# Kernel optimization log

Measured on AMD Instinct MI355X. Metric: run time of the kernel, lower is better.

The kernel has to match this reference:

```python
import jax, jax.numpy as jnp
import numpy as np

LN_EPS = 1e-5

def _ln(x, g, b):
    mu = x.mean(-1, keepdims=True)
    var = ((x - mu) ** 2).mean(-1, keepdims=True)
    return (x - mu) * jax.lax.rsqrt(var + LN_EPS) * g + b

def _gru(x, h, wih, whh, bih, bhh):
    # torch GRUCell: gates ordered (r, z, n)
    gi = x @ wih.T + bih
    gh = h @ whh.T + bhh
    ir, iz, inn = jnp.split(gi, 3, axis=-1)
    hr, hz, hn = jnp.split(gh, 3, axis=-1)
    r = jax.nn.sigmoid(ir + hr)
    z = jax.nn.sigmoid(iz + hz)
    n = jnp.tanh(inn + r * hn)
    return (1.0 - z) * n + z * h

def setup_inputs() -> dict:
    key = jax.random.key(0)
    ks = jax.random.split(key, 10)
    B, N, D, S, H = 64, 4096, 128, 8, 256
    w = D ** -0.5  # weight scale to keep activations sane
    return {
        'inputs': jax.random.normal(ks[0], (B, N, D), jnp.float32),
        'slot_noise': jax.random.normal(ks[1], (1, S, D), jnp.float32),
        'slots_mu': jax.random.normal(ks[2], (1, S, D), jnp.float32) * w,
        'slots_log_sigma': jnp.zeros((1, S, D), jnp.float32),
        'wq': jax.random.normal(ks[3], (D, D), jnp.float32) * w,
        'bq': jnp.zeros((D,), jnp.float32),
        'wk': jax.random.normal(ks[4], (D, D), jnp.float32) * w,
        'bk': jnp.zeros((D,), jnp.float32),
        'wv': jax.random.normal(ks[5], (D, D), jnp.float32) * w,
        'bv': jnp.zeros((D,), jnp.float32),
        'gru_wih': jax.random.normal(ks[6], (3 * D, D), jnp.float32) * w,
        'gru_whh': jax.random.normal(ks[7], (3 * D, D), jnp.float32) * w,
        'gru_bih': jnp.zeros((3 * D,), jnp.float32),
        'gru_bhh': jnp.zeros((3 * D,), jnp.float32),
        'ns_g': jnp.ones((D,), jnp.float32),
        'ns_b': jnp.zeros((D,), jnp.float32),
        'ni_g': jnp.ones((D,), jnp.float32),
        'ni_b': jnp.zeros((D,), jnp.float32),
        'mlp_ln_g': jnp.ones((D,), jnp.float32),
        'mlp_ln_b': jnp.zeros((D,), jnp.float32),
        'mlp_w1': jax.random.normal(ks[8], (H, D), jnp.float32) * w,
        'mlp_b1': jnp.zeros((H,), jnp.float32),
        'mlp_w2': jax.random.normal(ks[9], (D, H), jnp.float32) * (H ** -0.5),
        'mlp_b2': jnp.zeros((D,), jnp.float32),
    }

N_ITERS = 3

def reference(inputs, slot_noise, slots_mu, slots_log_sigma, wq, bq, wk, bk, wv, bv,
              gru_wih, gru_whh, gru_bih, gru_bhh, ns_g, ns_b, ni_g, ni_b,
              mlp_ln_g, mlp_ln_b, mlp_w1, mlp_b1, mlp_w2, mlp_b2):
    B, N, D = inputs.shape
    S = slots_mu.shape[1]
    slots = slots_mu + jnp.exp(slots_log_sigma) * slot_noise  # [1,S,D]
    slots = jnp.broadcast_to(slots, (B, S, D))
    x = _ln(inputs, ni_g, ni_b)
    k = x @ wk.T + bk  # [B,N,D]
    v = x @ wv.T + bv
    scale = 1.0 / jnp.sqrt(jnp.float32(D))
    for _ in range(N_ITERS):
        q = _ln(slots, ns_g, ns_b) @ wq.T + bq  # [B,S,D]
        logits = jnp.einsum('bnd,bsd->bns', k, q) * scale
        attn = jax.nn.softmax(logits, axis=-1)  # softmax over slots
        attn_norm = jnp.clip(attn.sum(axis=1, keepdims=True), 1e-8, None)
        slot_attn = attn / attn_norm
        updates = jnp.einsum('bns,bnd->bsd', slot_attn, v)
        slots = _gru(updates, slots, gru_wih, gru_whh, gru_bih, gru_bhh)
        h = jax.nn.gelu(_ln(slots, mlp_ln_g, mlp_ln_b) @ mlp_w1.T + mlp_b1, approximate=False)
        slots = slots + (h @ mlp_w2.T + mlp_b2)
    return slots
```

## Files before the change

### kernel.cpp

```cpp
#include <hip/hip_runtime.h>
#include <hip/hip_bf16.h>
#include <math.h>

#define Bn 64
#define Nn 4096
#define Dn 128
#define Sn 8
#define Hn 256
#define LN_EPS 1e-5f
#define QSCALE 0.08838834764831845f
#define NCHUNK 16

typedef __bf16 bf16x8 __attribute__((ext_vector_type(8)));
typedef float f32x4 __attribute__((ext_vector_type(4)));
typedef unsigned short ushort_t;

__device__ __forceinline__ float dot4(float4 a, float4 b) {
    return a.x*b.x + a.y*b.y + a.z*b.z + a.w*b.w;
}
__device__ __forceinline__ ushort_t f2bf(float f) {
    __bf16 b = (__bf16)f;
    ushort_t u; __builtin_memcpy(&u, &b, 2); return u;
}
__device__ __forceinline__ bf16x8 zero8() {
    bf16x8 z;
    #pragma unroll
    for (int i = 0; i < 8; ++i) z[i] = (__bf16)0.0f;
    return z;
}

__global__ void k_prep(const float* __restrict__ wk, const float* __restrict__ wv,
                       ushort_t* __restrict__ wallT,
                       const float* __restrict__ mu, const float* __restrict__ ls,
                       const float* __restrict__ noise, float* __restrict__ slots) {
    if (blockIdx.x < 128) {
        int o = blockIdx.x * 256 + threadIdx.x;
        int e = o & 7;
        int l = (o >> 3) & 15;
        int q = (o >> 7) & 3;
        int k = (o >> 9) & 3;
        int G = o >> 11;
        int row = G * 16 + l;
        int col = k * 32 + q * 8 + e;
        float f = (row < 128) ? wk[row * 128 + col] : wv[(row - 128) * 128 + col];
        wallT[o] = f2bf(f);
    } else {
        int i = (blockIdx.x - 128) * 256 + threadIdx.x;
        if (i < Sn * Dn) {
            float v = mu[i] + __expf(ls[i]) * noise[i];
            #pragma unroll 4
            for (int b = 0; b < Bn; ++b) slots[b * Sn * Dn + i] = v;
        }
    }
}

__global__ __launch_bounds__(512) void k_lnkv_mfma(
    const float* __restrict__ inp, const float* __restrict__ ni_g, const float* __restrict__ ni_b,
    const ushort_t* __restrict__ wallT, const float* __restrict__ bk, const float* __restrict__ bv,
    ushort_t* __restrict__ kout, ushort_t* __restrict__ vout)
{
    __shared__ ushort_t wsh[32768];
    const int t = threadIdx.x;
    const int lane = t & 63;
    const int w = t >> 6;
    const int l15 = lane & 15, q = lane >> 4;
    const int rowbase = blockIdx.x * 128;
    const int row = rowbase + w * 16 + l15;
    const int b_idx = rowbase >> 12;

    const float* xr = inp + (size_t)row * Dn + q * 8;
    float4 xv[8];
    #pragma unroll
    for (int c = 0; c < 4; ++c) {
        xv[2*c]   = *(const float4*)(xr + c * 32);
        xv[2*c+1] = *(const float4*)(xr + c * 32 + 4);
    }
    #pragma unroll
    for (int i = 0; i < 8; ++i) {
        int off = (i * 512 + t) * 8;
        *(bf16x8*)&wsh[off] = *(const bf16x8*)&wallT[off];
    }

    float s = 0.f, sq = 0.f;
    #pragma unroll
    for (int i = 0; i < 8; ++i) {
        float4 x4 = xv[i];
        s  += x4.x + x4.y + x4.z + x4.w;
        sq += x4.x*x4.x + x4.y*x4.y + x4.z*x4.z + x4.w*x4.w;
    }
    s  += __shfl_xor(s, 16);  s  += __shfl_xor(s, 32);
    sq += __shfl_xor(sq, 16); sq += __shfl_xor(sq, 32);
    float mu = s * (1.0f / 128.0f);
    float rs = rsqrtf(sq * (1.0f / 128.0f) - mu * mu + LN_EPS);

    bf16x8 xf[4];
    #pragma unroll
    for (int c = 0; c < 4; ++c) {
        const float* gp = ni_g + c * 32 + q * 8;
        const float* bp = ni_b + c * 32 + q * 8;
        float4 g0 = *(const float4*)gp, g1 = *(const float4*)(gp + 4);
        float4 b0 = *(const float4*)bp, b1 = *(const float4*)(bp + 4);
        bf16x8 f;
        f[0] = (__bf16)((xv[2*c].x   - mu) * rs * g0.x + b0.x);
        f[1] = (__bf16)((xv[2*c].y   - mu) * rs * g0.y + b0.y);
        f[2] = (__bf16)((xv[2*c].z   - mu) * rs * g0.z + b0.z);
        f[3] = (__bf16)((xv[2*c].w   - mu) * rs * g0.w + b0.w);
        f[4] = (__bf16)((xv[2*c+1].x - mu) * rs * g1.x + b1.x);
        f[5] = (__bf16)((xv[2*c+1].y - mu) * rs * g1.y + b1.y);
        f[6] = (__bf16)((xv[2*c+1].z - mu) * rs * g1.z + b1.z);
        f[7] = (__bf16)((xv[2*c+1].w - mu) * rs * g1.w + b1.w);
        xf[c] = f;
    }

    __syncthreads();

    const int nloc0 = (rowbase & 4095) + w * 16 + q * 4;
    #pragma unroll
    for (int ct = 0; ct < 16; ++ct) {
        bf16x8 af[4];
        #pragma unroll
        for (int k4 = 0; k4 < 4; ++k4)
            af[k4] = *(const bf16x8*)&wsh[((ct * 4 + k4) * 64 + lane) * 8];
        f32x4 acc = {0.f, 0.f, 0.f, 0.f};
        if (ct < 8) {
            #pragma unroll
            for (int k4 = 0; k4 < 4; ++k4)
                acc = __builtin_amdgcn_mfma_f32_16x16x32_bf16(af[k4], xf[k4], acc, 0, 0, 0);
            int d0 = ct * 16 + q * 4;
            float4 bia = *(const float4*)&bk[d0];
            ushort4 o = { f2bf(acc[0] + bia.x), f2bf(acc[1] + bia.y),
                          f2bf(acc[2] + bia.z), f2bf(acc[3] + bia.w) };
            size_t off = ((size_t)(((rowbase >> 4) + w) * 4 + (d0 >> 5)) * 64
                          + ((d0 >> 3) & 3) * 16 + l15) * 8 + (d0 & 7);
            *(ushort4*)&kout[off] = o;
        } else {
            #pragma unroll
            for (int k4 = 0; k4 < 4; ++k4)
                acc = __builtin_amdgcn_mfma_f32_16x16x32_bf16(xf[k4], af[k4], acc, 0, 0, 0);
            int dgrp = ct - 8;
            float bb = bv[dgrp * 16 + l15];
            ushort4 o = { f2bf(acc[0] + bb), f2bf(acc[1] + bb),
                          f2bf(acc[2] + bb), f2bf(acc[3] + bb) };
            size_t off = (((size_t)(b_idx * 8 + dgrp) * 128 + (nloc0 >> 5)) * 64
                          + ((nloc0 >> 3) & 3) * 16 + l15) * 8 + (nloc0 & 7);
            *(ushort4*)&vout[off] = o;
        }
    }
}

__global__ __launch_bounds__(256) void k_qproj2(
    const float* __restrict__ slots, const float* __restrict__ ns_g, const float* __restrict__ ns_b,
    const float* __restrict__ wq, const float* __restrict__ bq,
    ushort_t* __restrict__ qb)
{
    __shared__ float lnq[8][128];
    const int t = threadIdx.x;
    const int bs0 = blockIdx.x * 8;
    {
        int r = t >> 5, c = (t & 31) * 4;
        float4 x4 = *(const float4*)&slots[(size_t)(bs0 + r) * Dn + c];
        float s  = x4.x + x4.y + x4.z + x4.w;
        float sq = x4.x*x4.x + x4.y*x4.y + x4.z*x4.z + x4.w*x4.w;
        #pragma unroll
        for (int m = 1; m <= 16; m <<= 1) { s += __shfl_xor(s, m); sq += __shfl_xor(sq, m); }
        float mu = s * (1.0f / 128.0f);
        float rs = rsqrtf(sq * (1.0f / 128.0f) - mu * mu + LN_EPS);
        lnq[r][c+0] = (x4.x - mu) * rs * ns_g[c+0] + ns_b[c+0];
        lnq[r][c+1] = (x4.y - mu) * rs * ns_g[c+1] + ns_b[c+1];
        lnq[r][c+2] = (x4.z - mu) * rs * ns_g[c+2] + ns_b[c+2];
        lnq[r][c+3] = (x4.w - mu) * rs * ns_g[c+3] + ns_b[c+3];
    }
    __syncthreads();
    {
        int c = t & 127, rb = (t >> 7) * 4;
        const float* W = wq + (size_t)c * Dn;
        float acc[4] = {0.f, 0.f, 0.f, 0.f};
        for (int d = 0; d < 128; d += 4) {
            float4 w4 = *(const float4*)(W + d);
            #pragma unroll
            for (int rr = 0; rr < 4; ++rr) acc[rr] += dot4(w4, *(const float4*)&lnq[rb + rr][d]);
        }
        float bb = bq[c];
        #pragma unroll
        for (int rr = 0; rr < 4; ++rr)
            qb[(size_t)(bs0 + rb + rr) * Dn + c] = f2bf((acc[rr] + bb) * QSCALE);
    }
}

__global__ __launch_bounds__(512) void k_attn_mfma(
    const ushort_t* __restrict__ kbuf, const ushort_t* __restrict__ vtbuf,
    const ushort_t* __restrict__ qb,
    float* __restrict__ upart, float* __restrict__ npart)
{
    __shared__ float ush[8][8][128];
    __shared__ float nsh[8][8];
    __shared__ ushort_t psh[8][8][32];
    const int t = threadIdx.x;
    const int b = blockIdx.y;
    const int chunk = blockIdx.x;
    const int lane = t & 63;
    const int w = t >> 6;
    const int l15 = lane & 15, q = lane >> 4;

    bf16x8 aq[4];
    #pragma unroll
    for (int c = 0; c < 4; ++c) {
        bf16x8 z = zero8();
        if (l15 < 8)
            z = *(const bf16x8*)&qb[((size_t)b * Sn + l15) * Dn + c * 32 + q * 8];
        aq[c] = z;
    }

    const int n32 = chunk * 256 + w * 32;
    const int ng = n32 >> 4;
    const int nc = n32 >> 5;

    f32x4 lg2[2];
    #pragma unroll
    for (int T = 0; T < 2; ++T) {
        f32x4 lg = {0.f, 0.f, 0.f, 0.f};
        #pragma unroll
        for (int c = 0; c < 4; ++c) {
            bf16x8 kf = *(const bf16x8*)&kbuf[(((size_t)b * 256 + ng + T) * 4 + c) * 512 + lane * 8];
            lg = __builtin_amdgcn_mfma_f32_16x16x32_bf16(aq[c], kf, lg, 0, 0, 0);
        }
        lg2[T] = lg;
    }

    bf16x8 bvf[8];
    #pragma unroll
    for (int dg = 0; dg < 8; ++dg)
        bvf[dg] = *(const bf16x8*)&vtbuf[(((size_t)b * 8 + dg) * 128 + nc) * 512 + lane * 8];

    #pragma unroll
    for (int T = 0; T < 2; ++T) {
        f32x4 lg = lg2[T];
        float m = fmaxf(fmaxf(lg[0], lg[1]), fmaxf(lg[2], lg[3]));
        m = fmaxf(m, __shfl_xor(m, 16));
        float e0 = __expf(lg[0] - m);
        float e1 = __expf(lg[1] - m);
        float e2 = __expf(lg[2] - m);
        float e3 = __expf(lg[3] - m);
        float ss = (e0 + e1) + (e2 + e3);
        ss += __shfl_xor(ss, 16);
        float inv = 1.0f / ss;
        if (q < 2) {
            psh[w][q * 4 + 0][T * 16 + l15] = f2bf(e0 * inv);
            psh[w][q * 4 + 1][T * 16 + l15] = f2bf(e1 * inv);
            psh[w][q * 4 + 2][T * 16 + l15] = f2bf(e2 * inv);
            psh[w][q * 4 + 3][T * 16 + l15] = f2bf(e3 * inv);
        }
    }

    bf16x8 pa = zero8();
    if (l15 < 8)
        pa = *(const bf16x8*)&psh[w][l15][q * 8];

    float nacc = 0.f;
    #pragma unroll
    for (int e = 0; e < 8; ++e) nacc += (float)pa[e];

    f32x4 acc[8];
    #pragma unroll
    for (int dg = 0; dg < 8; ++dg) {
        acc[dg] = (f32x4){0.f, 0.f, 0.f, 0.f};
        acc[dg] = __builtin_amdgcn_mfma_f32_16x16x32_bf16(pa, bvf[dg], acc[dg], 0, 0, 0);
    }

    nacc += __shfl_xor(nacc, 16);
    nacc += __shfl_xor(nacc, 32);
    if (lane < 8) nsh[w][lane] = nacc;
    if (q < 2) {
        #pragma unroll
        for (int dg = 0; dg < 8; ++dg)
            #pragma unroll
            for (int r = 0; r < 4; ++r)
                ush[w][q * 4 + r][dg * 16 + l15] = acc[dg][r];
    }
    __syncthreads();
    if (t < 256) {
        int s = t >> 5, d0 = (t & 31) * 4;
        float4 sum = {0.f, 0.f, 0.f, 0.f};
        #pragma unroll
        for (int w8 = 0; w8 < 8; ++w8) {
            float4 vv = *(const float4*)&ush[w8][s][d0];
            sum.x += vv.x; sum.y += vv.y; sum.z += vv.z; sum.w += vv.w;
        }
        *(float4*)&upart[((size_t)chunk * 512 + b * 8 + s) * 128 + d0] = sum;
    }
    if (t < 8) {
        float sn = 0.f;
        #pragma unroll
        for (int w8 = 0; w8 < 8; ++w8) sn += nsh[w8][t];
        npart[chunk * 512 + b * 8 + t] = sn;
    }
}

__global__ __launch_bounds__(512) void k_update3(
    const float* __restrict__ slots,
    const float* __restrict__ upart, const float* __restrict__ npart,
    const float* __restrict__ wih, const float* __restrict__ whh,
    const float* __restrict__ bih, const float* __restrict__ bhh,
    const float* __restrict__ mlg, const float* __restrict__ mlb,
    const float* __restrict__ w1, const float* __restrict__ b1,
    const float* __restrict__ w2, const float* __restrict__ b2,
    const float* __restrict__ ns_g, const float* __restrict__ ns_b,
    const float* __restrict__ wq, const float* __restrict__ bq,
    float* __restrict__ outp, ushort_t* __restrict__ qb, int do_q)
{
    __shared__ float us[128];
    __shared__ float hs[128];
    __shared__ float gs[768];
    __shared__ float hnw[128];
    __shared__ float lns[128];
    __shared__ float h1s[256];
    const int t = threadIdx.x;
    const int bs = blockIdx.x;

    if (t < 128) {
        float u = 0.f;
        #pragma unroll
        for (int c = 0; c < NCHUNK; ++c) u += upart[((size_t)(c * 512 + bs)) * 128 + t];
        float nsum = 0.f;
        #pragma unroll
        for (int c = 0; c < NCHUNK; ++c) nsum += npart[c * 512 + bs];
        us[t] = u / fmaxf(nsum, 1e-8f);
        hs[t] = slots[(size_t)bs * Dn + t];
    }
    __syncthreads();

    #pragma unroll
    for (int jj = 0; jj < 2; ++jj) {
        int j = t + jj * 512;
        if (jj == 0 || t < 256) {
            const float* W = (j < 384) ? (wih + (size_t)j * Dn) : (whh + (size_t)(j - 384) * Dn);
            const float* X = (j < 384) ? us : hs;
            float a = 0.f;
            #pragma unroll 8
            for (int d = 0; d < 128; d += 4)
                a += dot4(*(const float4*)(W + d), *(const float4*)(X + d));
            gs[j] = a;
        }
    }
    __syncthreads();

    if (t < 64) {
        float hnew[2];
        #pragma unroll
        for (int e = 0; e < 2; ++e) {
            int i = t + e * 64;
            float ir = gs[i]       + bih[i],       hr = gs[384 + i] + bhh[i];
            float iz = gs[128 + i] + bih[128 + i], hz = gs[512 + i] + bhh[128 + i];
            float in_= gs[256 + i] + bih[256 + i], hn = gs[640 + i] + bhh[256 + i];
            float r = 1.0f / (1.0f + __expf(-(ir + hr)));
            float z = 1.0f / (1.0f + __expf(-(iz + hz)));
            float n = tanhf(in_ + r * hn);
            hnew[e] = (1.0f - z) * n + z * hs[i];
        }
        float s  = hnew[0] + hnew[1];
        float sq = hnew[0]*hnew[0] + hnew[1]*hnew[1];
        #pragma unroll
        for (int m = 1; m <= 32; m <<= 1) { s += __shfl_xor(s, m); sq += __shfl_xor(sq, m); }
        float mu = s * (1.0f / 128.0f);
        float rs = rsqrtf(sq * (1.0f / 128.0f) - mu * mu + LN_EPS);
        #pragma unroll
        for (int e = 0; e < 2; ++e) {
            int i = t + e * 64;
            hnw[i] = hnew[e];
            lns[i] = (hnew[e] - mu) * rs * mlg[i] + mlb[i];
        }
    }
    __syncthreads();

    {
        int h = t >> 1, half = t & 1;
        const float* W = w1 + (size_t)h * Dn + half * 64;
        const float* X = lns + half * 64;
        float a = 0.f;
        #pragma unroll 8
        for (int d = 0; d < 64; d += 4)
            a += dot4(*(const float4*)(W + d), *(const float4*)(X + d));
        a += __shfl_xor(a, 1);
        if (half == 0) {
            float x = a + b1[h];
            h1s[h] = 0.5f * x * (1.0f + erff(x * 0.70710678118654752f));
        }
    }
    __syncthreads();

    {
        int d = t >> 2, q4 = t & 3;
        const float* W = w2 + (size_t)d * Hn + q4 * 64;
        const float* X = h1s + q4 * 64;
        float a = 0.f;
        #pragma unroll 8
        for (int e = 0; e < 64; e += 4)
            a += dot4(*(const float4*)(W + e), *(const float4*)(X + e));
        a += __shfl_xor(a, 1);
        a += __shfl_xor(a, 2);
        if (q4 == 0) {
            float o = hnw[d] + a + b2[d];
            outp[(size_t)bs * Dn + d] = o;
            us[d] = o;
        }
    }
    if (do_q) {
        __syncthreads();
        if (t < 64) {
            float v0 = us[t], v1 = us[t + 64];
            float s  = v0 + v1;
            float sq = v0*v0 + v1*v1;
            #pragma unroll
            for (int m = 1; m <= 32; m <<= 1) { s += __shfl_xor(s, m); sq += __shfl_xor(sq, m); }
            float mu = s * (1.0f / 128.0f);
            float rs = rsqrtf(sq * (1.0f / 128.0f) - mu * mu + LN_EPS);
            lns[t]      = (v0 - mu) * rs * ns_g[t]      + ns_b[t];
            lns[t + 64] = (v1 - mu) * rs * ns_g[t + 64] + ns_b[t + 64];
        }
        __syncthreads();
        {
            int d = t >> 2, q4 = t & 3;
            const float* W = wq + (size_t)d * Dn + q4 * 32;
            const float* X = lns + q4 * 32;
            float a = 0.f;
            #pragma unroll 8
            for (int e = 0; e < 32; e += 4)
                a += dot4(*(const float4*)(W + e), *(const float4*)(X + e));
            a += __shfl_xor(a, 1);
            a += __shfl_xor(a, 2);
            if (q4 == 0)
                qb[(size_t)bs * Dn + d] = f2bf((a + bq[d]) * QSCALE);
        }
    }
}

extern "C" void kernel_launch(void* const* d_in, const int* in_sizes, int n_in,
                              void* d_out, int out_size, void* d_ws, size_t ws_size,
                              hipStream_t stream) {
    (void)in_sizes; (void)n_in; (void)out_size; (void)ws_size;
    const float* inputs   = (const float*)d_in[0];
    const float* noise    = (const float*)d_in[1];
    const float* slots_mu = (const float*)d_in[2];
    const float* slots_ls = (const float*)d_in[3];
    const float* wq  = (const float*)d_in[4];
    const float* bq  = (const float*)d_in[5];
    const float* wk  = (const float*)d_in[6];
    const float* bk  = (const float*)d_in[7];
    const float* wv  = (const float*)d_in[8];
    const float* bv  = (const float*)d_in[9];
    const float* gwih = (const float*)d_in[10];
    const float* gwhh = (const float*)d_in[11];
    const float* gbih = (const float*)d_in[12];
    const float* gbhh = (const float*)d_in[13];
    const float* ns_g = (const float*)d_in[14];
    const float* ns_b = (const float*)d_in[15];
    const float* ni_g = (const float*)d_in[16];
    const float* ni_b = (const float*)d_in[17];
    const float* mlg  = (const float*)d_in[18];
    const float* mlb  = (const float*)d_in[19];
    const float* mw1  = (const float*)d_in[20];
    const float* mb1  = (const float*)d_in[21];
    const float* mw2  = (const float*)d_in[22];
    const float* mb2  = (const float*)d_in[23];

    float* ws      = (float*)d_ws;
    float* slots   = ws;
    float* upart   = ws + 65536;
    float* npart   = ws + 1114112;
    ushort_t* qb    = (ushort_t*)(ws + 1122304);
    ushort_t* wallT = (ushort_t*)(ws + 1155072);
    ushort_t* kbuf  = (ushort_t*)(ws + 1171456);
    ushort_t* vtbuf = kbuf + 33554432;

    k_prep<<<132, 256, 0, stream>>>(wk, wv, wallT, slots_mu, slots_ls, noise, slots);
    k_lnkv_mfma<<<2048, 512, 0, stream>>>(inputs, ni_g, ni_b, wallT, bk, bv, kbuf, vtbuf);
    k_qproj2<<<64, 256, 0, stream>>>(slots, ns_g, ns_b, wq, bq, qb);
    for (int iter = 0; iter < 3; ++iter) {
        k_attn_mfma<<<dim3(NCHUNK, 64), 512, 0, stream>>>(kbuf, vtbuf, qb, upart, npart);
        float* outp = (iter == 2) ? (float*)d_out : slots;
        k_update3<<<512, 512, 0, stream>>>(slots, upart, npart, gwih, gwhh, gbih, gbhh,
                                           mlg, mlb, mw1, mb1, mw2, mb2, ns_g, ns_b, wq, bq,
                                           outp, qb, (iter == 2) ? 0 : 1);
    }
}
```

Baseline: 465.3 us.

## Fuse three attention/update iterations into one persistent kernel with per-batch flags

Replaces the six per-iteration launches (attention and slot update) with a single persistent kernel. Each batch is handled by 8 blocks that each process a chunk of N, publish partial sums, and synchronise through an atomic counter before every block redundantly runs the GRU/MLP/q-projection for its batch. This removes launch overhead and global q round-trips but duplicates the small update work eightfold and depends on all 512 blocks being co-resident to avoid deadlock.

```diff
diff --git a/kernel.cpp b/kernel.cpp
--- a/kernel.cpp
+++ b/kernel.cpp
@@ -9,12 +9,14 @@
 #define Hn 256
 #define LN_EPS 1e-5f
 #define QSCALE 0.08838834764831845f
-#define NCHUNK 16
 
 typedef __bf16 bf16x8 __attribute__((ext_vector_type(8)));
 typedef float f32x4 __attribute__((ext_vector_type(4)));
 typedef unsigned short ushort_t;
 
+#define AGENT_LD(p)      __hip_atomic_load((p), __ATOMIC_RELAXED, __HIP_MEMORY_SCOPE_AGENT)
+#define AGENT_ST(p, v)   __hip_atomic_store((p), (v), __ATOMIC_RELAXED, __HIP_MEMORY_SCOPE_AGENT)
+
 __device__ __forceinline__ float dot4(float4 a, float4 b) {
     return a.x*b.x + a.y*b.y + a.z*b.z + a.w*b.w;
 }
@@ -32,7 +34,8 @@
 __global__ void k_prep(const float* __restrict__ wk, const float* __restrict__ wv,
                        ushort_t* __restrict__ wallT,
                        const float* __restrict__ mu, const float* __restrict__ ls,
-                       const float* __restrict__ noise, float* __restrict__ slots) {
+                       const float* __restrict__ noise, float* __restrict__ slots,
+                       unsigned* __restrict__ flags) {
     if (blockIdx.x < 128) {
         int o = blockIdx.x * 256 + threadIdx.x;
         int e = o & 7;
@@ -45,6 +48,7 @@
         float f = (row < 128) ? wk[row * 128 + col] : wv[(row - 128) * 128 + col];
         wallT[o] = f2bf(f);
     } else {
+        if (blockIdx.x == 128 && threadIdx.x < 192) flags[threadIdx.x] = 0u;
         int i = (blockIdx.x - 128) * 256 + threadIdx.x;
         if (i < Sn * Dn) {
             float v = mu[i] + __expf(ls[i]) * noise[i];
@@ -187,118 +191,10 @@
     }
 }
 
-__global__ __launch_bounds__(512) void k_attn_mfma(
+__global__ __launch_bounds__(512, 4) void k_iter(
     const ushort_t* __restrict__ kbuf, const ushort_t* __restrict__ vtbuf,
-    const ushort_t* __restrict__ qb,
-    float* __restrict__ upart, float* __restrict__ npart)
-{
-    __shared__ float ush[8][8][128];
-    __shared__ float nsh[8][8];
-    __shared__ ushort_t psh[8][8][32];
-    const int t = threadIdx.x;
-    const int b = blockIdx.y;
-    const int chunk = blockIdx.x;
-    const int lane = t & 63;
-    const int w = t >> 6;
-    const int l15 = lane & 15, q = lane >> 4;
-
-    bf16x8 aq[4];
-    #pragma unroll
-    for (int c = 0; c < 4; ++c) {
-        bf16x8 z = zero8();
-        if (l15 < 8)
-            z = *(const bf16x8*)&qb[((size_t)b * Sn + l15) * Dn + c * 32 + q * 8];
-        aq[c] = z;
-    }
-
-    const int n32 = chunk * 256 + w * 32;
-    const int ng = n32 >> 4;
-    const int nc = n32 >> 5;
-
-    f32x4 lg2[2];
-    #pragma unroll
-    for (int T = 0; T < 2; ++T) {
-        f32x4 lg = {0.f, 0.f, 0.f, 0.f};
-        #pragma unroll
-        for (int c = 0; c < 4; ++c) {
-            bf16x8 kf = *(const bf16x8*)&kbuf[(((size_t)b * 256 + ng + T) * 4 + c) * 512 + lane * 8];
-            lg = __builtin_amdgcn_mfma_f32_16x16x32_bf16(aq[c], kf, lg, 0, 0, 0);
-        }
-        lg2[T] = lg;
-    }
-
-    bf16x8 bvf[8];
-    #pragma unroll
-    for (int dg = 0; dg < 8; ++dg)
-        bvf[dg] = *(const bf16x8*)&vtbuf[(((size_t)b * 8 + dg) * 128 + nc) * 512 + lane * 8];
-
-    #pragma unroll
-    for (int T = 0; T < 2; ++T) {
-        f32x4 lg = lg2[T];
-        float m = fmaxf(fmaxf(lg[0], lg[1]), fmaxf(lg[2], lg[3]));
-        m = fmaxf(m, __shfl_xor(m, 16));
-        float e0 = __expf(lg[0] - m);
-        float e1 = __expf(lg[1] - m);
-        float e2 = __expf(lg[2] - m);
-        float e3 = __expf(lg[3] - m);
-        float ss = (e0 + e1) + (e2 + e3);
-        ss += __shfl_xor(ss, 16);
-        float inv = 1.0f / ss;
-        if (q < 2) {
-            psh[w][q * 4 + 0][T * 16 + l15] = f2bf(e0 * inv);
-            psh[w][q * 4 + 1][T * 16 + l15] = f2bf(e1 * inv);
-            psh[w][q * 4 + 2][T * 16 + l15] = f2bf(e2 * inv);
-            psh[w][q * 4 + 3][T * 16 + l15] = f2bf(e3 * inv);
-        }
-    }
-
-    bf16x8 pa = zero8();
-    if (l15 < 8)
-        pa = *(const bf16x8*)&psh[w][l15][q * 8];
-
-    float nacc = 0.f;
-    #pragma unroll
-    for (int e = 0; e < 8; ++e) nacc += (float)pa[e];
-
-    f32x4 acc[8];
-    #pragma unroll
-    for (int dg = 0; dg < 8; ++dg) {
-        acc[dg] = (f32x4){0.f, 0.f, 0.f, 0.f};
-        acc[dg] = __builtin_amdgcn_mfma_f32_16x16x32_bf16(pa, bvf[dg], acc[dg], 0, 0, 0);
-    }
-
-    nacc += __shfl_xor(nacc, 16);
-    nacc += __shfl_xor(nacc, 32);
-    if (lane < 8) nsh[w][lane] = nacc;
-    if (q < 2) {
-        #pragma unroll
-        for (int dg = 0; dg < 8; ++dg)
-            #pragma unroll
-            for (int r = 0; r < 4; ++r)
-                ush[w][q * 4 + r][dg * 16 + l15] = acc[dg][r];
-    }
-    __syncthreads();
-    if (t < 256) {
-        int s = t >> 5, d0 = (t & 31) * 4;
-        float4 sum = {0.f, 0.f, 0.f, 0.f};
-        #pragma unroll
-        for (int w8 = 0; w8 < 8; ++w8) {
-            float4 vv = *(const float4*)&ush[w8][s][d0];
-            sum.x += vv.x; sum.y += vv.y; sum.z += vv.z; sum.w += vv.w;
-        }
-        *(float4*)&upart[((size_t)chunk * 512 + b * 8 + s) * 128 + d0] = sum;
-    }
-    if (t < 8) {
-        float sn = 0.f;
-        #pragma unroll
-        for (int w8 = 0; w8 < 8; ++w8) sn += nsh[w8][t];
-        npart[chunk * 512 + b * 8 + t] = sn;
-    }
-}
-
-__global__ __launch_bounds__(512) void k_update3(
-    const float* __restrict__ slots,
-    const float* __restrict__ upart, const float* __restrict__ npart,
+    const ushort_t* __restrict__ qb0, const float* __restrict__ slots,
+    float* __restrict__ upart, float* __restrict__ npart,
     const float* __restrict__ wih, const float* __restrict__ whh,
     const float* __restrict__ bih, const float* __restrict__ bhh,
     const float* __restrict__ mlg, const float* __restrict__ mlb,
@@ -306,130 +202,308 @@
     const float* __restrict__ w2, const float* __restrict__ b2,
     const float* __restrict__ ns_g, const float* __restrict__ ns_b,
     const float* __restrict__ wq, const float* __restrict__ bq,
-    float* __restrict__ outp, ushort_t* __restrict__ qb, int do_q)
+    float* __restrict__ outp, unsigned* __restrict__ flags)
 {
-    __shared__ float us[128];
-    __shared__ float hs[128];
-    __shared__ float gs[768];
-    __shared__ float hnw[128];
-    __shared__ float lns[128];
-    __shared__ float h1s[256];
+    __shared__ union {
+        struct { float ush[8][8][128]; ushort_t psh[8][8][32]; float nsh[8][8]; } at;
+        struct { float us[8][128]; float gs[8][768]; float hnw[8][128];
+                 float lns[8][128]; float h1s[8][256]; } up;
+    } sh;
+    __shared__ float hs[8][128];
+    __shared__ ushort_t qloc[8][128];
+
     const int t = threadIdx.x;
-    const int bs = blockIdx.x;
-
-    if (t < 128) {
-        float u = 0.f;
+    const int lane = t & 63;
+    const int w = t >> 6;
+    const int l15 = lane & 15, q = lane >> 4;
+    const int b  = blockIdx.x >> 3;
+    const int ch = blockIdx.x & 7;
+
+    #pragma unroll
+    for (int k2 = 0; k2 < 2; ++k2) {
+        int idx = t + k2 * 512;
+        int s = idx >> 7, d = idx & 127;
+        hs[s][d]   = slots[((size_t)b * 8 + s) * 128 + d];
+        qloc[s][d] = qb0[((size_t)b * 8 + s) * 128 + d];
+    }
+    __syncthreads();
+
+    for (int iter = 0; iter < 3; ++iter) {
+        float* up = upart + (((size_t)iter * 64 + b) * 8) * 1024;
+        float* np = npart + (((size_t)iter * 64 + b) * 8) * 8;
+
+        {
+            bf16x8 aq[4];
+            #pragma unroll
+            for (int c = 0; c < 4; ++c) {
+                bf16x8 z = zero8();
+                if (l15 < 8)
+                    z = *(const bf16x8*)&qloc[l15][c * 32 + q * 8];
+                aq[c] = z;
+            }
+
+            f32x4 acc[8];
+            #pragma unroll
+            for (int dg = 0; dg < 8; ++dg) acc[dg] = (f32x4){0.f, 0.f, 0.f, 0.f};
+            float nacc = 0.f;
+
+            #pragma unroll
+            for (int u = 0; u < 2; ++u) {
+                const int n32 = ch * 512 + w * 64 + u * 32;
+                const int ng = n32 >> 4;
+                const int nc = n32 >> 5;
+
+                f32x4 lg2[2];
+                #pragma unroll
+                for (int T = 0; T < 2; ++T) {
+                    f32x4 lg = {0.f, 0.f, 0.f, 0.f};
+                    #pragma unroll
+                    for (int c = 0; c < 4; ++c) {
+                        bf16x8 kf = *(const bf16x8*)&kbuf[(((size_t)b * 256 + ng + T) * 4 + c) * 512 + lane * 8];
+                        lg = __builtin_amdgcn_mfma_f32_16x16x32_bf16(aq[c], kf, lg, 0, 0, 0);
+                    }
+                    lg2[T] = lg;
+                }
+
+                bf16x8 bvf[8];
+                #pragma unroll
+                for (int dg = 0; dg < 8; ++dg)
+                    bvf[dg] = *(const bf16x8*)&vtbuf[(((size_t)b * 8 + dg) * 128 + nc) * 512 + lane * 8];
+
+                #pragma unroll
+                for (int T = 0; T < 2; ++T) {
+                    f32x4 lg = lg2[T];
+                    float m = fmaxf(fmaxf(lg[0], lg[1]), fmaxf(lg[2], lg[3]));
+                    m = fmaxf(m, __shfl_xor(m, 16));
+                    float e0 = __expf(lg[0] - m);
+                    float e1 = __expf(lg[1] - m);
+                    float e2 = __expf(lg[2] - m);
+                    float e3 = __expf(lg[3] - m);
+                    float ss = (e0 + e1) + (e2 + e3);
+                    ss += __shfl_xor(ss, 16);
+                    float inv = 1.0f / ss;
+                    if (q < 2) {
+                        sh.at.psh[w][q * 4 + 0][T * 16 + l15] = f2bf(e0 * inv);
+                        sh.at.psh[w][q * 4 + 1][T * 16 + l15] = f2bf(e1 * inv);
+                        sh.at.psh[w][q * 4 + 2][T * 16 + l15] = f2bf(e2 * inv);
+                        sh.at.psh[w][q * 4 + 3][T * 16 + l15] = f2bf(e3 * inv);
+                    }
+                }
+
+                bf16x8 pa = zero8();
+                if (l15 < 8)
+                    pa = *(const bf16x8*)&sh.at.psh[w][l15][q * 8];
+
+                #pragma unroll
+                for (int e = 0; e < 8; ++e) nacc += (float)pa[e];
+
+                #pragma unroll
+                for (int dg = 0; dg < 8; ++dg)
+                    acc[dg] = __builtin_amdgcn_mfma_f32_16x16x32_bf16(pa, bvf[dg], acc[dg], 0, 0, 0);
+            }
+
+            nacc += __shfl_xor(nacc, 16);
+            nacc += __shfl_xor(nacc, 32);
+            if (lane < 8) sh.at.nsh[w][lane] = nacc;
+            if (q < 2) {
+                #pragma unroll
+                for (int dg = 0; dg < 8; ++dg)
+                    #pragma unroll
+                    for (int r = 0; r < 4; ++r)
+                        sh.at.ush[w][q * 4 + r][dg * 16 + l15] = acc[dg][r];
+            }
+            __syncthreads();
+            if (t < 256) {
+                int s = t >> 5, d0 = (t & 31) * 4;
+                float4 sum = {0.f, 0.f, 0.f, 0.f};
+                #pragma unroll
+                for (int w8 = 0; w8 < 8; ++w8) {
+                    float4 vv = *(const float4*)&sh.at.ush[w8][s][d0];
+                    sum.x += vv.x; sum.y += vv.y; sum.z += vv.z; sum.w += vv.w;
+                }
+                float* dst = up + ((size_t)ch * 8 + s) * 128 + d0;
+                AGENT_ST(dst + 0, sum.x);
+                AGENT_ST(dst + 1, sum.y);
+                AGENT_ST(dst + 2, sum.z);
+                AGENT_ST(dst + 3, sum.w);
+            }
+            if (t < 8) {
+                float sn = 0.f;
+                #pragma unroll
+                for (int w8 = 0; w8 < 8; ++w8) sn += sh.at.nsh[w8][t];
+                AGENT_ST(np + ch * 8 + t, sn);
+            }
+        }
+
+        asm volatile("s_waitcnt vmcnt(0)" ::: "memory");
+        __syncthreads();
+        if (t == 0) {
+            unsigned* fl = &flags[iter * 64 + b];
+            __hip_atomic_fetch_add(fl, 1u, __ATOMIC_RELAXED, __HIP_MEMORY_SCOPE_AGENT);
+            while (__hip_atomic_load(fl, __ATOMIC_RELAXED, __HIP_MEMORY_SCOPE_AGENT) < 8u)
+                __builtin_amdgcn_s_sleep(2);
+        }
+        __syncthreads();
+
         #pragma unroll
-        for (int c = 0; c < NCHUNK; ++c) u += upart[((size_t)(c * 512 + bs)) * 128 + t];
-        float nsum = 0.f;
+        for (int k2 = 0; k2 < 2; ++k2) {
+            int idx = t + k2 * 512;
+            int s = idx >> 7, d = idx & 127;
+            float usum = 0.f, nsum = 0.f;
+            #pragma unroll
+            for (int c = 0; c < 8; ++c) {
+                usum += AGENT_LD(up + ((size_t)c * 8 + s) * 128 + d);
+                nsum += AGENT_LD(np + c * 8 + s);
+            }
+            sh.up.us[s][d] = usum / fmaxf(nsum, 1e-8f);
+        }
+        __syncthreads();
+
         #pragma unroll
-        for (int c = 0; c < NCHUNK; ++c) nsum += npart[c * 512 + bs];
-        us[t] = u / fmaxf(nsum, 1e-8f);
-        hs[t] = slots[(size_t)bs * Dn + t];
-    }
-    __syncthreads();
-
-    #pragma unroll
-    for (int jj = 0; jj < 2; ++jj) {
-        int j = t + jj * 512;
-        if (jj == 0 || t < 256) {
-            const float* W = (j < 384) ? (wih + (size_t)j * Dn) : (whh + (size_t)(j - 384) * Dn);
-            const float* X = (j < 384) ? us : hs;
-            float a = 0.f;
-            #pragma unroll 8
-            for (int d = 0; d < 128; d += 4)
-                a += dot4(*(const float4*)(W + d), *(const float4*)(X + d));
-            gs[j] = a;
-        }
-    }
-    __syncthreads();
-
-    if (t < 64) {
-        float hnew[2];
-        #pragma unroll
-        for (int e = 0; e < 2; ++e) {
-            int i = t + e * 64;
-            float ir = gs[i]       + bih[i],       hr = gs[384 + i] + bhh[i];
-            float iz = gs[128 + i] + bih[128 + i], hz = gs[512 + i] + bhh[128 + i];
-            float in_= gs[256 + i] + bih[256 + i], hn = gs[640 + i] + bhh[256 + i];
-            float r = 1.0f / (1.0f + __expf(-(ir + hr)));
-            float z = 1.0f / (1.0f + __expf(-(iz + hz)));
-            float n = tanhf(in_ + r * hn);
-            hnew[e] = (1.0f - z) * n + z * hs[i];
-        }
-        float s  = hnew[0] + hnew[1];
-        float sq = hnew[0]*hnew[0] + hnew[1]*hnew[1];
-        #pragma unroll
-        for (int m = 1; m <= 32; m <<= 1) { s += __shfl_xor(s, m); sq += __shfl_xor(sq, m); }
-        float mu = s * (1.0f / 128.0f);
-        float rs = rsqrtf(sq * (1.0f / 128.0f) - mu * mu + LN_EPS);
-        #pragma unroll
-        for (int e = 0; e < 2; ++e) {
-            int i = t + e * 64;
-            hnw[i] = hnew[e];
-            lns[i] = (hnew[e] - mu) * rs * mlg[i] + mlb[i];
-        }
-    }
-    __syncthreads();
-
-    {
-        int h = t >> 1, half = t & 1;
-        const float* W = w1 + (size_t)h * Dn + half * 64;
-        const float* X = lns + half * 64;
-        float a = 0.f;
-        #pragma unroll 8
-        for (int d = 0; d < 64; d += 4)
-            a += dot4(*(const float4*)(W + d), *(const float4*)(X + d));
-        a += __shfl_xor(a, 1);
-        if (half == 0) {
-            float x = a + b1[h];
-            h1s[h] = 0.5f * x * (1.0f + erff(x * 0.70710678118654752f));
-        }
-    }
-    __syncthreads();
-
-    {
-        int d = t >> 2, q4 = t & 3;
-        const float* W = w2 + (size_t)d * Hn + q4 * 64;
-        const float* X = h1s + q4 * 64;
-        float a = 0.f;
-        #pragma unroll 8
-        for (int e = 0; e < 64; e += 4)
-            a += dot4(*(const float4*)(W + e), *(const float4*)(X + e));
-        a += __shfl_xor(a, 1);
-        a += __shfl_xor(a, 2);
-        if (q4 == 0) {
-            float o = hnw[d] + a + b2[d];
-            outp[(size_t)bs * Dn + d] = o;
-            us[d] = o;
-        }
-    }
-    if (do_q) {
+        for (int jj = 0; jj < 2; ++jj) {
+            int j = t + jj * 512;
+            if (jj == 0 || t < 256) {
+                const float* W = (j < 384) ? (wih + (size_t)j * Dn) : (whh + (size_t)(j - 384) * Dn);
+                const float* X0 = (j < 384) ? &sh.up.us[0][0] : &hs[0][0];
+                float a[8] = {0.f,0.f,0.f,0.f,0.f,0.f,0.f,0.f};
+                #pragma unroll 4
+                for (int d = 0; d < 128; d += 4) {
+                    float4 w4 = *(const float4*)(W + d);
+                    #pragma unroll
+                    for (int s = 0; s < 8; ++s)
+                        a[s] += dot4(w4, *(const float4*)(X0 + s * 128 + d));
+                }
+                #pragma unroll
+                for (int s = 0; s < 8; ++s) sh.up.gs[s][j] = a[s];
+            }
+        }
         __syncthreads();
-        if (t < 64) {
-            float v0 = us[t], v1 = us[t + 64];
-            float s  = v0 + v1;
-            float sq = v0*v0 + v1*v1;
-            #pragma unroll
-            for (int m = 1; m <= 32; m <<= 1) { s += __shfl_xor(s, m); sq += __shfl_xor(sq, m); }
-            float mu = s * (1.0f / 128.0f);
-            float rs = rsqrtf(sq * (1.0f / 128.0f) - mu * mu + LN_EPS);
-            lns[t]      = (v0 - mu) * rs * ns_g[t]      + ns_b[t];
-            lns[t + 64] = (v1 - mu) * rs * ns_g[t + 64] + ns_b[t + 64];
+
+        {
+            const int s = w;
+            float hnew[2];
+            #pragma unroll
+            for (int e = 0; e < 2; ++e) {
+                int i = lane + e * 64;
+                float ir = sh.up.gs[s][i]       + bih[i],       hr = sh.up.gs[s][384 + i] + bhh[i];
+                float iz = sh.up.gs[s][128 + i] + bih[128 + i], hz = sh.up.gs[s][512 + i] + bhh[128 + i];
+                float in_= sh.up.gs[s][256 + i] + bih[256 + i], hn = sh.up.gs[s][640 + i] + bhh[256 + i];
+                float r = 1.0f / (1.0f + __expf(-(ir + hr)));
+                float z = 1.0f / (1.0f + __expf(-(iz + hz)));
+                float n = tanhf(in_ + r * hn);
+                hnew[e] = (1.0f - z) * n + z * hs[s][i];
+            }
+            float sm  = hnew[0] + hnew[1];
+            float sq2 = hnew[0]*hnew[0] + hnew[1]*hnew[1];
+            #pragma unroll
+            for (int m = 1; m <= 32; m <<= 1) { sm += __shfl_xor(sm, m); sq2 += __shfl_xor(sq2, m); }
+            float mu = sm * (1.0f / 128.0f);
+            float rs = rsqrtf(sq2 * (1.0f / 128.0f) - mu * mu + LN_EPS);
+            #pragma unroll
+            for (int e = 0; e < 2; ++e) {
+                int i = lane + e * 64;
+                sh.up.hnw[s][i] = hnew[e];
+                sh.up.lns[s][i] = (hnew[e] - mu) * rs * mlg[i] + mlb[i];
+            }
         }
         __syncthreads();
+
         {
-            int d = t >> 2, q4 = t & 3;
-            const float* W = wq + (size_t)d * Dn + q4 * 32;
-            const float* X = lns + q4 * 32;
-            float a = 0.f;
-            #pragma unroll 8
-            for (int e = 0; e < 32; e += 4)
-                a += dot4(*(const float4*)(W + e), *(const float4*)(X + e));
-            a += __shfl_xor(a, 1);
-            a += __shfl_xor(a, 2);
-            if (q4 == 0)
-                qb[(size_t)bs * Dn + d] = f2bf((a + bq[d]) * QSCALE);
+            int h = t >> 1, half = t & 1;
+            const float* W = w1 + (size_t)h * Dn + half * 64;
+            const float* X = &sh.up.lns[0][0] + half * 64;
+            float a[8] = {0.f,0.f,0.f,0.f,0.f,0.f,0.f,0.f};
+            #pragma unroll 4
+            for (int d = 0; d < 64; d += 4) {
+                float4 w4 = *(const float4*)(W + d);
+                #pragma unroll
+                for (int s = 0; s < 8; ++s)
+                    a[s] += dot4(w4, *(const float4*)(X + s * 128 + d));
+            }
+            #pragma unroll
+            for (int s = 0; s < 8; ++s) a[s] += __shfl_xor(a[s], 1);
+            if (half == 0) {
+                float bb = b1[h];
+                #pragma unroll
+                for (int s = 0; s < 8; ++s) {
+                    float x = a[s] + bb;
+                    sh.up.h1s[s][h] = 0.5f * x * (1.0f + erff(x * 0.70710678118654752f));
+                }
+            }
+        }
+        __syncthreads();
+
+        {
+            int d2 = t >> 2, kq = t & 3;
+            const float* W = w2 + (size_t)d2 * Hn + kq * 64;
+            const float* X = &sh.up.h1s[0][0] + kq * 64;
+            float a[8] = {0.f,0.f,0.f,0.f,0.f,0.f,0.f,0.f};
+            #pragma unroll 4
+            for (int e = 0; e < 64; e += 4) {
+                float4 w4 = *(const float4*)(W + e);
+                #pragma unroll
+                for (int s = 0; s < 8; ++s)
+                    a[s] += dot4(w4, *(const float4*)(X + s * 256 + e));
+            }
+            #pragma unroll
+            for (int s = 0; s < 8; ++s) {
+                a[s] += __shfl_xor(a[s], 1);
+                a[s] += __shfl_xor(a[s], 2);
+            }
+            if (kq == 0) {
+                float bb = b2[d2];
+                #pragma unroll
+                for (int s = 0; s < 8; ++s) {
+                    float o = sh.up.hnw[s][d2] + a[s] + bb;
+                    if (iter == 2) {
+                        if (ch == 0) outp[((size_t)b * 8 + s) * 128 + d2] = o;
+                    } else {
+                        hs[s][d2] = o;
+                    }
+                }
+            }
+        }
+
+        if (iter < 2) {
+            __syncthreads();
+            {
+                const int s = w;
+                float v0 = hs[s][lane], v1 = hs[s][lane + 64];
+                float sm  = v0 + v1;
+                float sq2 = v0*v0 + v1*v1;
+                #pragma unroll
+                for (int m = 1; m <= 32; m <<= 1) { sm += __shfl_xor(sm, m); sq2 += __shfl_xor(sq2, m); }
+                float mu = sm * (1.0f / 128.0f);
+                float rs = rsqrtf(sq2 * (1.0f / 128.0f) - mu * mu + LN_EPS);
+                sh.up.lns[s][lane]      = (v0 - mu) * rs * ns_g[lane]      + ns_b[lane];
+                sh.up.lns[s][lane + 64] = (v1 - mu) * rs * ns_g[lane + 64] + ns_b[lane + 64];
+            }
+            __syncthreads();
+            {
+                int c = t >> 2, kq = t & 3;
+                const float* W = wq + (size_t)c * Dn + kq * 32;
+                const float* X = &sh.up.lns[0][0] + kq * 32;
+                float a[8] = {0.f,0.f,0.f,0.f,0.f,0.f,0.f,0.f};
+                #pragma unroll 4
+                for (int e = 0; e < 32; e += 4) {
+                    float4 w4 = *(const float4*)(W + e);
+                    #pragma unroll
+                    for (int s = 0; s < 8; ++s)
+                        a[s] += dot4(w4, *(const float4*)(X + s * 128 + e));
+                }
+                #pragma unroll
+                for (int s = 0; s < 8; ++s) {
+                    a[s] += __shfl_xor(a[s], 1);
+                    a[s] += __shfl_xor(a[s], 2);
+                }
+                if (kq == 0) {
+                    float bb = bq[c];
+                    #pragma unroll
+                    for (int s = 0; s < 8; ++s)
+                        qloc[s][c] = f2bf((a[s] + bb) * QSCALE);
+                }
+            }
+            __syncthreads();
         }
     }
 }
@@ -466,20 +540,18 @@
     float* ws      = (float*)d_ws;
     float* slots   = ws;
     float* upart   = ws + 65536;
-    float* npart   = ws + 1114112;
-    ushort_t* qb    = (ushort_t*)(ws + 1122304);
-    ushort_t* wallT = (ushort_t*)(ws + 1155072);
-    ushort_t* kbuf  = (ushort_t*)(ws + 1171456);
+    float* npart   = ws + 1638400;
+    ushort_t* qb    = (ushort_t*)(ws + 1650688);
+    ushort_t* wallT = (ushort_t*)(ws + 1683456);
+    unsigned* flags = (unsigned*)(ws + 1699840);
+    ushort_t* kbuf  = (ushort_t*)(ws + 1700352);
     ushort_t* vtbuf = kbuf + 33554432;
 
-    k_prep<<<132, 256, 0, stream>>>(wk, wv, wallT, slots_mu, slots_ls, noise, slots);
+    k_prep<<<132, 256, 0, stream>>>(wk, wv, wallT, slots_mu, slots_ls, noise, slots, flags);
     k_lnkv_mfma<<<2048, 512, 0, stream>>>(inputs, ni_g, ni_b, wallT, bk, bv, kbuf, vtbuf);
     k_qproj2<<<64, 256, 0, stream>>>(slots, ns_g, ns_b, wq, bq, qb);
-    for (int iter = 0; iter < 3; ++iter) {
-        k_attn_mfma<<<dim3(NCHUNK, 64), 512, 0, stream>>>(kbuf, vtbuf, qb, upart, npart);
-        float* outp = (iter == 2) ? (float*)d_out : slots;
-        k_update3<<<512, 512, 0, stream>>>(slots, upart, npart, gwih, gwhh, gbih, gbhh,
-                                           mlg, mlb, mw1, mb1, mw2, mb2, ns_g, ns_b, wq, bq,
-                                           outp, qb, (iter == 2) ? 0 : 1);
-    }
-}
+    k_iter<<<512, 512, 0, stream>>>(kbuf, vtbuf, qb, slots, upart, npart,
+                                    gwih, gwhh, gbih, gbhh, mlg, mlb, mw1, mb1,
+                                    mw2, mb2, ns_g, ns_b, wq, bq,
+                                    (float*)d_out, flags);
+}
```

Measured after the change: 638.9 us. +37.3%, slower.
